# Performance work log

Hardware: AMD Instinct MI355X
Metric: run time of the kernel (lower is better)

The kernel has to match this reference:

```python
import jax, jax.numpy as jnp
import numpy as np

STRIDE = 2.0      # MTCNN.STRIDE
CELLSIZE = 12.0   # MTCNN.CELLSIZE
SCALE = 0.5       # pyramid scale for this level
SCORE_T = 0.6     # threshold[0]
IOU_T = 0.5       # nms threshold ('union' method)
K = 2048          # fixed candidate budget (jit-friendly replacement for tf.where)


def setup_inputs() -> dict:
    key = jax.random.key(0)
    k1, k2 = jax.random.split(key)
    probs = jax.random.uniform(k1, (8, 768, 768), dtype=jnp.float32)          # PNet probs[..., 1]
    deviations = jax.random.normal(k2, (8, 768, 768, 4), dtype=jnp.float32) * 0.1  # PNet reg
    return {"probs": probs, "deviations": deviations}


def _decode_grid(H, W):
    # getBBox: pos = tf.where(...); here the full dense grid of candidate positions.
    ys, xs = jnp.meshgrid(jnp.arange(H, dtype=jnp.float32),
                          jnp.arange(W, dtype=jnp.float32), indexing='ij')
    pos = jnp.stack([ys, xs], axis=-1)                       # [H, W, 2] (row, col) like tf.where
    ul = jnp.round((pos * STRIDE + 1.0) / SCALE)             # upper_left
    dr = jnp.round((pos * STRIDE + CELLSIZE - 1.0 + 1.0) / SCALE)  # down_right
    return jnp.concatenate([ul, dr], axis=-1).reshape(-1, 4)  # [H*W, 4]


def _nms_keep(boxes, valid, iou_t):
    # boxes sorted descending by score; greedy suppression identical to the
    # original while-loop: highest unsuppressed survivor kills later boxes with IoU >= t.
    ul = boxes[:, 0:2]
    dr = boxes[:, 2:4]
    hw = dr - ul + 1.0
    area = hw[:, 0] * hw[:, 1]                                # [K]
    iul = jnp.maximum(ul[:, None, :], ul[None, :, :])         # [K, K, 2]
    idr = jnp.minimum(dr[:, None, :], dr[None, :, :])
    ihw = jnp.maximum(idr - iul + 1.0, 0.0)
    inter = ihw[..., 0] * ihw[..., 1]                         # [K, K]
    iou = inter / (area[:, None] + area[None, :] - inter)     # 'union' method
    n = boxes.shape[0]
    idx = jnp.arange(n)

    def body(i, supp):
        keep_i = valid[i] & (~supp[i])
        row = (iou[i] >= iou_t) & (idx > i) & keep_i
        return supp | row

    supp = jax.lax.fori_loop(0, n, body, jnp.zeros(n, dtype=bool))
    return valid & (~supp)


def reference(probs, deviations):
    B, H, W = probs.shape
    grid_boxes = _decode_grid(H, W)                           # [H*W, 4]
    scores = probs.reshape(B, -1)                             # [B, H*W]
    dev = deviations.reshape(B, -1, 4)                        # [B, H*W, 4]

    # threshold mask (tf.where(probs >= t)) expressed as masked top-k selection
    valid0 = scores >= SCORE_T
    masked = jnp.where(valid0, scores, -1.0)
    top_s, top_i = jax.lax.top_k(masked, K)                   # [B, K]
    top_boxes = grid_boxes[top_i]                             # [B, K, 4]
    top_dev = jnp.take_along_axis(dev, top_i[..., None], axis=1)  # [B, K, 4]
    valid = top_s >= SCORE_T

    keep = jax.vmap(lambda b, v: _nms_keep(b, v, IOU_T))(top_boxes, valid)  # [B, K] bool

    # applyDeviation
    hw = top_boxes[..., 2:4] - top_boxes[..., 0:2]
    refined = top_boxes + top_dev * jnp.concatenate([hw, hw], axis=-1)
    # toSquare
    rhw = refined[..., 2:4] - refined[..., 0:2]
    length = jnp.max(rhw, axis=-1, keepdims=True)
    center = refined[..., 0:2] + rhw * 0.5
    sq_ul = center - 0.5 * jnp.concatenate([length, length], axis=-1)
    sq_dr = sq_ul + jnp.concatenate([length, length], axis=-1)
    sq = jnp.concatenate([sq_ul, sq_dr], axis=-1)
    # clip to image extent [1, img_dim - 1]
    img_dim = jnp.ceil((H * STRIDE + CELLSIZE) / SCALE)
    sq = jnp.clip(sq, 1.0, img_dim - 1.0)

    keepf = keep.astype(probs.dtype)
    out = jnp.concatenate([sq * keepf[..., None], (top_s * keepf)[..., None]], axis=-1)  # [B, K, 5]
    return out
```

## Files before the change

kernel.cpp:

```cpp
#include <hip/hip_runtime.h>
#include <stdint.h>

#define W 768
#define NPROB (768*768)
#define NB 8
#define NBINS 2048
#define CAP 4096
#define TOPK 2048
#define SCORE_THR 0.6f
#define SUBS 32
#define SEG (NPROB/SUBS)
#define PER4 (SEG/4)

#define HPART_OFF  0
#define HPART_BYTES (NB*SUBS*NBINS*2)
#define BUCKET_OFF (HPART_OFF + HPART_BYTES)
#define BUCKET_BYTES (NB*(size_t)SUBS*SEG*8)
#define WS_TOTAL   (BUCKET_OFF + BUCKET_BYTES)

__device__ __forceinline__ unsigned score_bin(unsigned fb) {
    return (fb >> 12) & 0x7FFu;
}

__global__ __launch_bounds__(256) void scatter_kernel(
    const float* __restrict__ probs, unsigned* __restrict__ hpart32,
    unsigned long long* __restrict__ bucket)
{
    __shared__ unsigned lh[NBINS];
    __shared__ unsigned cur[NBINS];
    __shared__ unsigned csum[256];
    __shared__ unsigned sB0;
    const int b = blockIdx.y, hs = blockIdx.x, tid = threadIdx.x;

    for (int i = tid; i < NBINS; i += 256) lh[i] = 0;
    if (tid == 0) sB0 = 0;
    __syncthreads();
    const float4* p = (const float4*)(probs + (size_t)b * NPROB) + (size_t)hs * PER4;
    for (int i = tid; i < PER4; i += 256) {
        float4 v = p[i];
        if (v.x >= SCORE_THR) atomicAdd(&lh[score_bin(__float_as_uint(v.x))], 1u);
        if (v.y >= SCORE_THR) atomicAdd(&lh[score_bin(__float_as_uint(v.y))], 1u);
        if (v.z >= SCORE_THR) atomicAdd(&lh[score_bin(__float_as_uint(v.z))], 1u);
        if (v.w >= SCORE_THR) atomicAdd(&lh[score_bin(__float_as_uint(v.w))], 1u);
    }
    __syncthreads();
    {
        unsigned* gh = hpart32 + (size_t)(b * SUBS + hs) * (NBINS / 2);
        for (int i = tid; i < NBINS / 2; i += 256)
            gh[i] = (lh[2 * i] & 0xFFFFu) | (lh[2 * i + 1] << 16);
    }
    unsigned s = 0;
    #pragma unroll
    for (int i = 0; i < 8; ++i) s += lh[tid * 8 + i];
    csum[tid] = s;
    __syncthreads();
    for (int off = 1; off < 256; off <<= 1) {
        unsigned v = (tid + off < 256) ? csum[tid + off] : 0u;
        __syncthreads();
        csum[tid] += v;
        __syncthreads();
    }
    unsigned run = csum[tid];
    unsigned localB0 = 0;
    #pragma unroll
    for (int i = 0; i < 8; ++i) {
        unsigned B = tid * 8 + i;
        if (run >= TOPK) localB0 = B;
        cur[B] = run - lh[B];
        run -= lh[B];
    }
    if (localB0) atomicMax(&sB0, localB0);
    __syncthreads();
    float thrF = __uint_as_float(0x3F000000u | (sB0 << 12));
    if (thrF < SCORE_THR) thrF = SCORE_THR;

    unsigned long long* dst = bucket + (size_t)(b * SUBS + hs) * SEG;
    int base_elem = hs * SEG;
    for (int i = tid; i < PER4; i += 256) {
        float4 v = p[i];
        int ei = base_elem + i * 4;
        float sv[4] = {v.x, v.y, v.z, v.w};
        #pragma unroll
        for (int c = 0; c < 4; ++c) {
            float s2 = sv[c];
            if (s2 >= thrF) {
                unsigned fb = __float_as_uint(s2);
                unsigned pos = atomicAdd(&cur[score_bin(fb)], 1u);
                unsigned idx = (unsigned)(ei + c);
                dst[pos] = ((unsigned long long)fb << 32) | (unsigned)(~idx);
            }
        }
    }
}

__device__ __forceinline__ unsigned suffix_scan1024(unsigned v, unsigned* wtot, int tid) {
    int lane = tid & 63, wv = tid >> 6;
    unsigned s = v;
    #pragma unroll
    for (int d = 1; d < 64; d <<= 1) {
        unsigned t = __shfl_down(s, d, 64);
        if (lane + d < 64) s += t;
    }
    if (lane == 0) wtot[wv] = s;
    __syncthreads();
    if (tid < 16) {
        unsigned t = wtot[tid];
        #pragma unroll
        for (int d = 1; d < 16; d <<= 1) {
            unsigned u2 = __shfl_down(t, d, 64);
            if (tid + d < 16) t += u2;
        }
        wtot[tid] = t;
    }
    __syncthreads();
    unsigned higher = (wv + 1 < 16) ? wtot[wv + 1] : 0u;
    return s + higher;
}
__device__ __forceinline__ unsigned prefix_scan1024(unsigned v, unsigned* wtot, int tid) {
    int lane = tid & 63, wv = tid >> 6;
    unsigned s = v;
    #pragma unroll
    for (int d = 1; d < 64; d <<= 1) {
        unsigned t = __shfl_up(s, d, 64);
        if (lane >= d) s += t;
    }
    if (lane == 63) wtot[wv] = s;
    __syncthreads();
    if (tid < 16) {
        unsigned t = wtot[tid];
        #pragma unroll
        for (int d = 1; d < 16; d <<= 1) {
            unsigned u2 = __shfl_up(t, d, 64);
            if (tid >= d) t += u2;
        }
        wtot[tid] = t;
    }
    __syncthreads();
    unsigned lower = (wv > 0) ? wtot[wv - 1] : 0u;
    return s + lower;
}

union UA {
    unsigned long long keysR[CAP];
    struct {
        unsigned rowcnt[W];
        unsigned rowstart[W + 1];
        unsigned rowcur[W];
        unsigned rowlist[CAP];
        unsigned char state[TOPK];
        int changed;
    } nb;
};

__global__ __launch_bounds__(1024) void finish_kernel(
    const float* __restrict__ dev4, const unsigned* __restrict__ hpart32,
    const unsigned long long* __restrict__ bucket, float* __restrict__ out)
{
    __shared__ unsigned p2[NBINS + 1];
    __shared__ unsigned h2[NBINS];
    __shared__ unsigned wtot[17];
    __shared__ unsigned long long keysS[CAP];
    __shared__ UA u;
    __shared__ unsigned sj[SUBS];
    __shared__ unsigned basej[SUBS + 1];
    __shared__ unsigned sbstar, sshift, sfbase;
    const int b = blockIdx.x, tid = threadIdx.x;

    unsigned c0 = 0, c1 = 0;
    for (int j = 0; j < SUBS; ++j) {
        unsigned pr = hpart32[(size_t)(b * SUBS + j) * (NBINS / 2) + tid];
        c0 += pr & 0xFFFFu;
        c1 += pr >> 16;
    }
    if (tid == 0) sbstar = 0;
    unsigned suf = suffix_scan1024(c0 + c1, wtot, tid);
    p2[2 * tid] = suf;
    p2[2 * tid + 1] = suf - c0;
    if (tid == 0) p2[NBINS] = 0;
    __syncthreads();
    {
        int B0 = 2 * tid, B1 = 2 * tid + 1;
        if (p2[B0] >= TOPK && p2[B0 + 1] < TOPK) sbstar = (unsigned)B0;
        if (p2[B1] >= TOPK && p2[B1 + 1] < TOPK) sbstar = (unsigned)B1;
    }
    __syncthreads();
    const unsigned bstar = sbstar;
    const unsigned Tfull = p2[bstar];
    const unsigned T = Tfull < CAP ? Tfull : CAP;
    const int nvalid = (int)(T < TOPK ? T : TOPK);

    {
        int j = tid >> 5, lane = tid & 31;
        unsigned s = 0;
        const unsigned* hp = hpart32 + (size_t)(b * SUBS + j) * (NBINS / 2);
        for (unsigned pi = (bstar >> 1) + lane; pi < NBINS / 2; pi += 32) {
            unsigned pr = hp[pi];
            unsigned lo = pr & 0xFFFFu, hi = pr >> 16;
            s += ((2 * pi) >= bstar ? lo : 0u) + hi;
        }
        #pragma unroll
        for (int d = 16; d > 0; d >>= 1) s += __shfl_down(s, d, 32);
        if (lane == 0) sj[j] = s;
    }
    __syncthreads();
    if (tid == 0) {
        unsigned acc = 0;
        for (int j = 0; j < SUBS; ++j) { basej[j] = acc; acc += sj[j]; }
        basej[SUBS] = acc;
        unsigned nb2 = 0x800u - bstar;
        unsigned sft = 0;
        while (((nb2 << 12) >> sft) > (unsigned)NBINS) ++sft;
        sshift = sft;
        sfbase = (0x3F000u + bstar) << 12;
    }
    __syncthreads();
    const unsigned shift = sshift, fbase = sfbase;

    for (unsigned i = tid; i < T; i += 1024) {
        int lo = 0, hi = SUBS - 1;
        while (lo < hi) { int mid = (lo + hi + 1) >> 1; if (basej[mid] <= i) lo = mid; else hi = mid - 1; }
        u.keysR[i] = bucket[(size_t)(b * SUBS + lo) * SEG + (i - basej[lo])];
    }
    for (int i = tid; i < NBINS; i += 1024) h2[i] = 0;
    __syncthreads();

    for (unsigned i = tid; i < T; i += 1024) {
        unsigned fb = (unsigned)(u.keysR[i] >> 32);
        atomicAdd(&h2[(fb - fbase) >> shift], 1u);
    }
    __syncthreads();
    {
        unsigned d0 = h2[2 * tid], d1 = h2[2 * tid + 1];
        unsigned sf = suffix_scan1024(d0 + d1, wtot, tid);
        p2[2 * tid] = sf;
        p2[2 * tid + 1] = sf - d0;
        if (tid == 0) p2[NBINS] = 0;
    }
    __syncthreads();
    for (int i = tid; i < NBINS; i += 1024) h2[i] = p2[i + 1];
    __syncthreads();

    for (unsigned i = tid; i < T; i += 1024) {
        unsigned long long key = u.keysR[i];
        unsigned fb = (unsigned)(key >> 32);
        unsigned pos = atomicAdd(&h2[(fb - fbase) >> shift], 1u);
        keysS[pos] = key;
    }
    __syncthreads();

    unsigned myr[4], myidx[4];
    unsigned long long mykey[4];
    #pragma unroll
    for (int q = 0; q < 4; ++q) {
        unsigned pos = tid + q * 1024;
        myr[q] = 0xFFFFFFFFu;
        mykey[q] = 0; myidx[q] = 0;
        if (pos < T) {
            unsigned long long key = keysS[pos];
            unsigned fb = (unsigned)(key >> 32);
            unsigned B = (fb - fbase) >> shift;
            unsigned st = p2[B + 1], en = p2[B];
            unsigned r = st;
            for (unsigned i = st; i < en; ++i) r += (keysS[i] > key);
            if (r < (unsigned)nvalid) {
                myr[q] = r; mykey[q] = key; myidx[q] = ~(unsigned)key;
            }
        }
    }
    __syncthreads();

    for (int i = tid; i < W; i += 1024) u.nb.rowcnt[i] = 0;
    for (int i = tid; i < TOPK; i += 1024) u.nb.state[i] = 2;
    __syncthreads();
    #pragma unroll
    for (int q = 0; q < 4; ++q)
        if (myr[q] != 0xFFFFFFFFu) atomicAdd(&u.nb.rowcnt[myidx[q] / W], 1u);
    __syncthreads();
    {
        unsigned c = (tid < W) ? u.nb.rowcnt[tid] : 0u;
        unsigned incl = prefix_scan1024(c, wtot, tid);
        if (tid < W) { u.nb.rowstart[tid + 1] = incl; u.nb.rowcur[tid] = incl - c; }
        if (tid == 0) u.nb.rowstart[0] = 0;
    }
    __syncthreads();
    #pragma unroll
    for (int q = 0; q < 4; ++q)
        if (myr[q] != 0xFFFFFFFFu) {
            unsigned y = myidx[q] / W, x = myidx[q] % W;
            unsigned pos = atomicAdd(&u.nb.rowcur[y], 1u);
            u.nb.rowlist[pos] = (x << 12) | myr[q];
        }
    __syncthreads();

    unsigned long long l0[4] = {0,0,0,0}, l1[4] = {0,0,0,0};
    int nc[4] = {0,0,0,0};
    #pragma unroll
    for (int q = 0; q < 4; ++q) {
        if (myr[q] != 0xFFFFFFFFu) {
            unsigned y = myidx[q] / W, x = myidx[q] % W;
            int c2 = 0;
            unsigned long long a0 = 0, a1 = 0;
            #pragma unroll
            for (int dy = -1; dy <= 1; ++dy) {
                unsigned yy = y + (unsigned)dy;
                if (yy < (unsigned)W) {
                    unsigned s0 = u.nb.rowstart[yy], e0 = u.nb.rowstart[yy + 1];
                    for (unsigned i = s0; i < e0; ++i) {
                        unsigned e = u.nb.rowlist[i];
                        unsigned xx = e >> 12, rr = e & 0xFFFu;
                        if ((xx - x + 1u) <= 2u && rr < myr[q]) {
                            if (c2 < 4)      a0 |= (unsigned long long)rr << (c2 * 16);
                            else if (c2 < 8) a1 |= (unsigned long long)rr << ((c2 - 4) * 16);
                            c2++;
                        }
                    }
                }
            }
            if (c2 > 8) c2 = 8;
            l0[q] = a0; l1[q] = a1; nc[q] = c2;
            u.nb.state[myr[q]] = (c2 == 0) ? 1 : 0;
        }
    }
    __syncthreads();

    while (true) {
        if (tid == 0) u.nb.changed = 0;
        __syncthreads();
        bool ch = false;
        #pragma unroll
        for (int q = 0; q < 4; ++q) {
            if (myr[q] != 0xFFFFFFFFu && u.nb.state[myr[q]] == 0) {
                bool anyK = false, anyU = false;
                int c = nc[q];
                #pragma unroll
                for (int l = 0; l < 8; ++l) {
                    if (l < c) {
                        unsigned rr = (l < 4)
                            ? (unsigned)((l0[q] >> (l * 16)) & 0xFFFFu)
                            : (unsigned)((l1[q] >> ((l - 4) * 16)) & 0xFFFFu);
                        unsigned char st = u.nb.state[rr];
                        anyK |= (st == 1);
                        anyU |= (st == 0);
                    }
                }
                if (anyK)      { u.nb.state[myr[q]] = 2; ch = true; }
                else if (!anyU){ u.nb.state[myr[q]] = 1; ch = true; }
            }
        }
        if (ch) u.nb.changed = 1;
        __syncthreads();
        if (u.nb.changed == 0) break;
        __syncthreads();
    }

    for (int r = nvalid + tid; r < TOPK; r += 1024) {
        float* op = out + ((size_t)b * TOPK + r) * 5;
        op[0] = 0.f; op[1] = 0.f; op[2] = 0.f; op[3] = 0.f; op[4] = 0.f;
    }
    #pragma unroll
    for (int q = 0; q < 4; ++q) {
        if (myr[q] != 0xFFFFFFFFu) {
            unsigned r = myr[q];
            float o0 = 0.f, o1 = 0.f, o2 = 0.f, o3 = 0.f, o4 = 0.f;
            if (u.nb.state[r] == 1) {
                unsigned idx = myidx[q];
                float sc = __uint_as_float((unsigned)(mykey[q] >> 32));
                int y = (int)(idx / W), x = (int)(idx % W);
                const float4 d = ((const float4*)dev4)[(size_t)b * NPROB + idx];
                float b0 = (float)(4 * y + 2);
                float b1 = (float)(4 * x + 2);
                float b2 = (float)(4 * y + 24);
                float b3 = (float)(4 * x + 24);
                float r0 = b0 + d.x * 22.0f;
                float r1 = b1 + d.y * 22.0f;
                float r2 = b2 + d.z * 22.0f;
                float r3 = b3 + d.w * 22.0f;
                float rh = r2 - r0, rw = r3 - r1;
                float len = fmaxf(rh, rw);
                float c0v = r0 + rh * 0.5f, c1v = r1 + rw * 0.5f;
                float u0 = c0v - 0.5f * len, u1 = c1v - 0.5f * len;
                float v0 = u0 + len, v1 = u1 + len;
                o0 = fminf(fmaxf(u0, 1.0f), 3095.0f);
                o1 = fminf(fmaxf(u1, 1.0f), 3095.0f);
                o2 = fminf(fmaxf(v0, 1.0f), 3095.0f);
                o3 = fminf(fmaxf(v1, 1.0f), 3095.0f);
                o4 = sc;
            }
            float* op = out + ((size_t)b * TOPK + r) * 5;
            op[0] = o0; op[1] = o1; op[2] = o2; op[3] = o3; op[4] = o4;
        }
    }
}

extern "C" void kernel_launch(void* const* d_in, const int* in_sizes, int n_in,
                              void* d_out, int out_size, void* d_ws, size_t ws_size,
                              hipStream_t stream) {
    (void)in_sizes; (void)n_in; (void)out_size;
    if (ws_size < (size_t)WS_TOTAL) return;

    const float* probs = (const float*)d_in[0];
    const float* devs  = (const float*)d_in[1];
    float* out = (float*)d_out;
    char* ws = (char*)d_ws;

    unsigned* hpart32 = (unsigned*)(ws + HPART_OFF);
    unsigned long long* bucket = (unsigned long long*)(ws + BUCKET_OFF);

    scatter_kernel<<<dim3(SUBS, NB), 256, 0, stream>>>(probs, hpart32, bucket);
    finish_kernel<<<NB, 1024, 0, stream>>>(devs, hpart32, bucket, out);
}
```

Baseline: 43.53 us.

## Fuse scatter and finish kernels using last-block flag synchronization

Merges the histogram/scatter pass and the per-batch finish pass into one kernel of 256 blocks of 1024 threads. The last sub-block of each batch spin-waits on release/acquire flags from its 31 siblings before doing the top-k, NMS and output work. This removes one kernel launch and the gap between launches, and reuses shared memory through a union. In exchange the scatter phase now runs at 1024 threads per block with heavy shared-memory use, so fewer blocks fit per CU. The spin-wait is only safe if all sibling blocks get scheduled before or alongside the waiter, and it relies on the flag workspace starting at zero or being reset.

```diff
diff --git a/kernel.cpp b/kernel.cpp
--- a/kernel.cpp
+++ b/kernel.cpp
@@ -11,86 +11,18 @@
 #define SUBS 32
 #define SEG (NPROB/SUBS)
 #define PER4 (SEG/4)
+#define MAGIC 0x4B1DC0DEu
 
 #define HPART_OFF  0
 #define HPART_BYTES (NB*SUBS*NBINS*2)
 #define BUCKET_OFF (HPART_OFF + HPART_BYTES)
 #define BUCKET_BYTES (NB*(size_t)SUBS*SEG*8)
-#define WS_TOTAL   (BUCKET_OFF + BUCKET_BYTES)
+#define FLAG_OFF   (BUCKET_OFF + BUCKET_BYTES)
+#define FLAG_BYTES (NB*SUBS*4)
+#define WS_TOTAL   (FLAG_OFF + FLAG_BYTES)
 
 __device__ __forceinline__ unsigned score_bin(unsigned fb) {
     return (fb >> 12) & 0x7FFu;
-}
-
-__global__ __launch_bounds__(256) void scatter_kernel(
-    const float* __restrict__ probs, unsigned* __restrict__ hpart32,
-    unsigned long long* __restrict__ bucket)
-{
-    __shared__ unsigned lh[NBINS];
-    __shared__ unsigned cur[NBINS];
-    __shared__ unsigned csum[256];
-    __shared__ unsigned sB0;
-    const int b = blockIdx.y, hs = blockIdx.x, tid = threadIdx.x;
-
-    for (int i = tid; i < NBINS; i += 256) lh[i] = 0;
-    if (tid == 0) sB0 = 0;
-    __syncthreads();
-    const float4* p = (const float4*)(probs + (size_t)b * NPROB) + (size_t)hs * PER4;
-    for (int i = tid; i < PER4; i += 256) {
-        float4 v = p[i];
-        if (v.x >= SCORE_THR) atomicAdd(&lh[score_bin(__float_as_uint(v.x))], 1u);
-        if (v.y >= SCORE_THR) atomicAdd(&lh[score_bin(__float_as_uint(v.y))], 1u);
-        if (v.z >= SCORE_THR) atomicAdd(&lh[score_bin(__float_as_uint(v.z))], 1u);
-        if (v.w >= SCORE_THR) atomicAdd(&lh[score_bin(__float_as_uint(v.w))], 1u);
-    }
-    __syncthreads();
-    {
-        unsigned* gh = hpart32 + (size_t)(b * SUBS + hs) * (NBINS / 2);
-        for (int i = tid; i < NBINS / 2; i += 256)
-            gh[i] = (lh[2 * i] & 0xFFFFu) | (lh[2 * i + 1] << 16);
-    }
-    unsigned s = 0;
-    #pragma unroll
-    for (int i = 0; i < 8; ++i) s += lh[tid * 8 + i];
-    csum[tid] = s;
-    __syncthreads();
-    for (int off = 1; off < 256; off <<= 1) {
-        unsigned v = (tid + off < 256) ? csum[tid + off] : 0u;
-        __syncthreads();
-        csum[tid] += v;
-        __syncthreads();
-    }
-    unsigned run = csum[tid];
-    unsigned localB0 = 0;
-    #pragma unroll
-    for (int i = 0; i < 8; ++i) {
-        unsigned B = tid * 8 + i;
-        if (run >= TOPK) localB0 = B;
-        cur[B] = run - lh[B];
-        run -= lh[B];
-    }
-    if (localB0) atomicMax(&sB0, localB0);
-    __syncthreads();
-    float thrF = __uint_as_float(0x3F000000u | (sB0 << 12));
-    if (thrF < SCORE_THR) thrF = SCORE_THR;
-
-    unsigned long long* dst = bucket + (size_t)(b * SUBS + hs) * SEG;
-    int base_elem = hs * SEG;
-    for (int i = tid; i < PER4; i += 256) {
-        float4 v = p[i];
-        int ei = base_elem + i * 4;
-        float sv[4] = {v.x, v.y, v.z, v.w};
-        #pragma unroll
-        for (int c = 0; c < 4; ++c) {
-            float s2 = sv[c];
-            if (s2 >= thrF) {
-                unsigned fb = __float_as_uint(s2);
-                unsigned pos = atomicAdd(&cur[score_bin(fb)], 1u);
-                unsigned idx = (unsigned)(ei + c);
-                dst[pos] = ((unsigned long long)fb << 32) | (unsigned)(~idx);
-            }
-        }
-    }
 }
 
 __device__ __forceinline__ unsigned suffix_scan1024(unsigned v, unsigned* wtot, int tid) {
@@ -140,7 +72,8 @@
     return s + lower;
 }
 
-union UA {
+union BigU {
+    struct { unsigned lh[NBINS]; unsigned cur[NBINS]; } sc;
     unsigned long long keysR[CAP];
     struct {
         unsigned rowcnt[W];
@@ -152,28 +85,92 @@
     } nb;
 };
 
-__global__ __launch_bounds__(1024) void finish_kernel(
-    const float* __restrict__ dev4, const unsigned* __restrict__ hpart32,
-    const unsigned long long* __restrict__ bucket, float* __restrict__ out)
+__global__ __launch_bounds__(1024) void fused_kernel(
+    const float* __restrict__ probs, const float* __restrict__ dev4,
+    unsigned* __restrict__ hpart32, unsigned long long* __restrict__ bucket,
+    unsigned* __restrict__ flags, float* __restrict__ out)
 {
+    __shared__ BigU u;
+    __shared__ unsigned long long keysS[CAP];
     __shared__ unsigned p2[NBINS + 1];
     __shared__ unsigned h2[NBINS];
     __shared__ unsigned wtot[17];
-    __shared__ unsigned long long keysS[CAP];
-    __shared__ UA u;
     __shared__ unsigned sj[SUBS];
     __shared__ unsigned basej[SUBS + 1];
-    __shared__ unsigned sbstar, sshift, sfbase;
-    const int b = blockIdx.x, tid = threadIdx.x;
-
-    unsigned c0 = 0, c1 = 0;
+    __shared__ unsigned sB0, sbstar, sshift, sfbase;
+    const int bid = blockIdx.x, tid = threadIdx.x;
+    const int b = bid >> 5, hs = bid & 31;
+
+    for (int i = tid; i < NBINS; i += 1024) u.sc.lh[i] = 0;
+    if (tid == 0) sB0 = 0;
+    __syncthreads();
+    const float4* p = (const float4*)(probs + (size_t)b * NPROB) + (size_t)hs * PER4;
+    for (int i = tid; i < PER4; i += 1024) {
+        float4 v = p[i];
+        if (v.x >= SCORE_THR) atomicAdd(&u.sc.lh[score_bin(__float_as_uint(v.x))], 1u);
+        if (v.y >= SCORE_THR) atomicAdd(&u.sc.lh[score_bin(__float_as_uint(v.y))], 1u);
+        if (v.z >= SCORE_THR) atomicAdd(&u.sc.lh[score_bin(__float_as_uint(v.z))], 1u);
+        if (v.w >= SCORE_THR) atomicAdd(&u.sc.lh[score_bin(__float_as_uint(v.w))], 1u);
+    }
+    __syncthreads();
+    unsigned c0 = u.sc.lh[2 * tid], c1 = u.sc.lh[2 * tid + 1];
+    hpart32[(size_t)(b * SUBS + hs) * (NBINS / 2) + tid] = (c0 & 0xFFFFu) | (c1 << 16);
+    unsigned suf = suffix_scan1024(c0 + c1, wtot, tid);
+    u.sc.cur[2 * tid] = suf - c0;
+    u.sc.cur[2 * tid + 1] = suf - c0 - c1;
+    unsigned lb0 = 0;
+    if (suf >= TOPK) lb0 = 2 * tid;
+    if (suf - c0 >= TOPK) lb0 = 2 * tid + 1;
+    if (lb0) atomicMax(&sB0, lb0);
+    __syncthreads();
+    float thrF = __uint_as_float(0x3F000000u | (sB0 << 12));
+    if (thrF < SCORE_THR) thrF = SCORE_THR;
+
+    unsigned long long* dst = bucket + (size_t)(b * SUBS + hs) * SEG;
+    int base_elem = hs * SEG;
+    for (int i = tid; i < PER4; i += 1024) {
+        float4 v = p[i];
+        int ei = base_elem + i * 4;
+        float sv[4] = {v.x, v.y, v.z, v.w};
+        #pragma unroll
+        for (int c = 0; c < 4; ++c) {
+            float s2 = sv[c];
+            if (s2 >= thrF) {
+                unsigned fb = __float_as_uint(s2);
+                unsigned pos = atomicAdd(&u.sc.cur[score_bin(fb)], 1u);
+                unsigned idx = (unsigned)(ei + c);
+                dst[pos] = ((unsigned long long)fb << 32) | (unsigned)(~idx);
+            }
+        }
+    }
+    __syncthreads();
+
+    if (hs != SUBS - 1) {
+        if (tid == 0) {
+            __threadfence();
+            __hip_atomic_store(&flags[b * SUBS + hs], MAGIC,
+                               __ATOMIC_RELEASE, __HIP_MEMORY_SCOPE_AGENT);
+        }
+        return;
+    }
+    if (tid < SUBS - 1) {
+        while (__hip_atomic_load(&flags[b * SUBS + tid],
+                                 __ATOMIC_ACQUIRE, __HIP_MEMORY_SCOPE_AGENT) != MAGIC)
+            __builtin_amdgcn_s_sleep(8);
+        __hip_atomic_store(&flags[b * SUBS + tid], 0u,
+                           __ATOMIC_RELAXED, __HIP_MEMORY_SCOPE_AGENT);
+    }
+    __syncthreads();
+    __threadfence();
+
+    c0 = 0; c1 = 0;
     for (int j = 0; j < SUBS; ++j) {
         unsigned pr = hpart32[(size_t)(b * SUBS + j) * (NBINS / 2) + tid];
         c0 += pr & 0xFFFFu;
         c1 += pr >> 16;
     }
     if (tid == 0) sbstar = 0;
-    unsigned suf = suffix_scan1024(c0 + c1, wtot, tid);
+    suf = suffix_scan1024(c0 + c1, wtot, tid);
     p2[2 * tid] = suf;
     p2[2 * tid + 1] = suf - c0;
     if (tid == 0) p2[NBINS] = 0;
@@ -405,7 +402,7 @@
 
     unsigned* hpart32 = (unsigned*)(ws + HPART_OFF);
     unsigned long long* bucket = (unsigned long long*)(ws + BUCKET_OFF);
-
-    scatter_kernel<<<dim3(SUBS, NB), 256, 0, stream>>>(probs, hpart32, bucket);
-    finish_kernel<<<NB, 1024, 0, stream>>>(devs, hpart32, bucket, out);
+    unsigned* flags = (unsigned*)(ws + FLAG_OFF);
+
+    fused_kernel<<<NB * SUBS, 1024, 0, stream>>>(probs, devs, hpart32, bucket, flags, out);
 }
```

After: 62.56 us. 43.7% more time.
